# Optimization experiments

Hardware: AMD Instinct MI355X
Metric: run time of the kernel (lower is better)

## Reference

```python
import jax, jax.numpy as jnp
import numpy as np


@jax.custom_vjp
def binarize_ste(x):
    return jnp.sign(x)


def _binarize_fwd(x):
    return jnp.sign(x), None


def _binarize_bwd(_, g):
    # straight-through estimator: pass gradient through, clamped to [-1, 1]
    return (jnp.clip(g, -1.0, 1.0),)


binarize_ste.defvjp(_binarize_fwd, _binarize_bwd)


def setup_inputs() -> dict:
    key = jax.random.key(0)
    kx, kw = jax.random.split(key)
    x = jax.random.normal(kx, (32, 128, 64, 64), dtype=jnp.float32)  # NCHW
    weight = jax.random.normal(kw, (256, 128, 3, 3), dtype=jnp.float32)  # OIHW
    return {"x": x, "weight": weight}


def reference(x, weight):
    w_bin = binarize_ste(weight)  # +/-1 (0 where weight==0, matching torch.sign)
    out = jax.lax.conv_general_dilated(
        x, w_bin,
        window_strides=(1, 1),
        padding=((1, 1), (1, 1)),
        dimension_numbers=("NCHW", "OIHW", "NCHW"),
    )
    return out
```

## Files before the change

### kernel.cpp

```cpp
#include <hip/hip_runtime.h>
#include <hip/hip_bf16.h>


typedef short bf16x8 __attribute__((ext_vector_type(8)));
typedef float f32x4 __attribute__((ext_vector_type(4)));

#define XT_ELEMS (32 * 66 * 66 * 128)
#define XT_BYTES (XT_ELEMS * 2)

__device__ __forceinline__ void glds16(const void* g, const void* l) {
    __builtin_amdgcn_global_load_lds(
        (const __attribute__((address_space(1))) void*)g,
        (__attribute__((address_space(3))) void*)l, 16, 0, 0);
}

__global__ void prep_w_kernel(const float* __restrict__ w,
                              __hip_bfloat16* __restrict__ wm) {
    int tid = blockIdx.x * 256 + threadIdx.x;
    int o = tid / 1152;
    int r = tid - o * 1152;
    int j = r >> 7;
    int c = r & 127;
    float v = w[o * 1152 + c * 9 + j];
    float s = (v > 0.f) ? 1.f : ((v < 0.f) ? -1.f : 0.f);
    wm[tid] = __float2bfloat16(s);
}

__global__ void transpose_x_kernel(const float* __restrict__ x,
                                   __hip_bfloat16* __restrict__ xt) {
    __shared__ short tl[64 * 130];
    const int t = threadIdx.x;
    const int n = blockIdx.x >> 6;
    const int h = blockIdx.x & 63;
    const float* xp = x + (size_t)n * 524288 + h * 64;
    for (int i = t; i < 8192; i += 256) {
        int w = i & 63, c = i >> 6;
        tl[w * 130 + c] = (short)__bfloat16_as_ushort(__float2bfloat16(xp[c * 4096 + w]));
    }
    uint* xtn = (uint*)(xt + (size_t)n * 66 * 66 * 128);
    {
        int row = h + 1;
        if (t < 64)       xtn[(row * 66 + 0) * 64 + t] = 0u;
        else if (t < 128) xtn[(row * 66 + 65) * 64 + (t - 64)] = 0u;
    }
    if (h == 0)  for (int i = t; i < 66 * 64; i += 256) xtn[i] = 0u;
    if (h == 63) for (int i = t; i < 66 * 64; i += 256) xtn[65 * 66 * 64 + i] = 0u;
    __syncthreads();
    uint* xo = (uint*)(xt + ((size_t)(n * 66 + h + 1) * 66 + 1) * 128);
    for (int i = t; i < 4096; i += 256) {
        int c2 = i & 63;
        int w = i >> 6;
        xo[w * 64 + c2] = *(const uint*)(tl + w * 130 + c2 * 2);
    }
}

__global__ __launch_bounds__(256, 2) void gemm_kernel(
    const __hip_bfloat16* __restrict__ xt,
    const __hip_bfloat16* __restrict__ wm,
    float* __restrict__ out) {
    __shared__ short As[128 * 64];
    __shared__ short Bw[2112 * 8];

    const int t = threadIdx.x;
    const int lane = t & 63;
    const int wv = t >> 6;
    const int px_blk = blockIdx.x;
    const int o_blk = blockIdx.y;
    const int n = px_blk >> 4;
    const int h0 = (px_blk & 15) * 4;

    const int wo = (wv & 1) * 64;
    const int wp = (wv >> 1) * 128;
    const int wpr = wp >> 6;
    const int l15 = lane & 15;
    const int quad = lane >> 4;
    const int srow = lane >> 3;
    const int sseg = lane & 7;

    const short* wmS = (const short*)wm + (o_blk * 128) * 1152;
    const short* xtS = (const short*)xt;

    f32x4 acc[4][8] = {};

    for (int cc = 0; cc < 128; cc += 64) {
        for (int kh = 0; kh < 3; ++kh) {
            const short* xw = xtS + ((size_t)(n * 66 + h0 + kh) * 66) * 128;
#pragma unroll
            for (int i = 0; i < 9; ++i) {
                int bidx = i * 4 + wv;
                if (bidx < 33) {
                    int l = bidx * 64 + lane;
                    int cell = l >> 3;
                    int q = l & 7;
                    int s = q ^ (cell & 7);
                    glds16(xw + cell * 128 + cc + s * 8, Bw + bidx * 512);
                }
            }
            for (int kw = 0; kw < 3; ++kw) {
                const int j = kh * 3 + kw;
#pragma unroll
                for (int i = 0; i < 4; ++i) {
                    int r0 = wv * 32 + i * 8;
                    int r = r0 + srow;
                    int segl = sseg ^ (r & 7);
                    glds16(wmS + r * 1152 + j * 128 + cc + segl * 8,
                           As + r0 * 64);
                }
                __syncthreads();
#pragma unroll
                for (int kf = 0; kf < 2; ++kf) {
                    bf16x8 a[4], b[8];
#pragma unroll
                    for (int i = 0; i < 4; ++i) {
                        int o = wo + i * 16 + l15;
                        int seg = (kf * 4 + quad) ^ (o & 7);
                        a[i] = *(const bf16x8*)(As + o * 64 + seg * 8);
                    }
#pragma unroll
                    for (int i = 0; i < 8; ++i) {
                        int cell = (wpr + (i >> 2)) * 66 + (i & 3) * 16 + l15 + kw;
                        int seg = (kf * 4 + quad) ^ (cell & 7);
                        b[i] = *(const bf16x8*)(Bw + cell * 64 + seg * 8);
                    }
#pragma unroll
                    for (int i = 0; i < 4; ++i)
#pragma unroll
                        for (int jj = 0; jj < 8; ++jj)
                            acc[i][jj] = __builtin_amdgcn_mfma_f32_16x16x32_bf16(
                                a[i], b[jj], acc[i][jj], 0, 0, 0);
                }
                __syncthreads();
            }
        }
    }

    const int Pbase = px_blk * 256 + wp;
#pragma unroll
    for (int i = 0; i < 4; ++i) {
#pragma unroll
        for (int jj = 0; jj < 8; ++jj) {
            const int P = Pbase + jj * 16 + l15;
            const int hw = P & 4095;
            float* op = out + (size_t)n * 1048576 + hw;
#pragma unroll
            for (int r = 0; r < 4; ++r) {
                const int o = o_blk * 128 + wo + i * 16 + quad * 4 + r;
                op[(size_t)o * 4096] = acc[i][jj][r];
            }
        }
    }
}

extern "C" void kernel_launch(void* const* d_in, const int* in_sizes, int n_in,
                              void* d_out, int out_size, void* d_ws, size_t ws_size,
                              hipStream_t stream) {
    const float* x = (const float*)d_in[0];
    const float* w = (const float*)d_in[1];
    float* out = (float*)d_out;
    __hip_bfloat16* xt = (__hip_bfloat16*)d_ws;
    __hip_bfloat16* wm = (__hip_bfloat16*)((char*)d_ws + XT_BYTES);

    prep_w_kernel<<<1152, 256, 0, stream>>>(w, wm);
    transpose_x_kernel<<<2048, 256, 0, stream>>>(x, xt);
    gemm_kernel<<<dim3(512, 2), 256, 0, stream>>>(xt, wm, out);
}
```

Baseline: 249.0 us.

## Load weights directly from global into registers and drop LDS A staging

The weight prep kernel now writes binarized weights in a fragment-friendly layout, so each lane can load its MFMA A operand straight from global memory and the LDS As buffer goes away. This removes the per-kw LDS staging of A and two of the three barriers per kh. Block indices are also remapped to change L2 locality across images. In exchange, the global weight loads are now exposed in the inner loop instead of being hidden behind LDS, and each wave fetches its own weights directly, which adds latency risk.

```diff
diff --git a/kernel.cpp b/kernel.cpp
--- a/kernel.cpp
+++ b/kernel.cpp
@@ -17,11 +17,11 @@
 __global__ void prep_w_kernel(const float* __restrict__ w,
                               __hip_bfloat16* __restrict__ wm) {
     int tid = blockIdx.x * 256 + threadIdx.x;
-    int o = tid / 1152;
-    int r = tid - o * 1152;
-    int j = r >> 7;
-    int c = r & 127;
-    float v = w[o * 1152 + c * 9 + j];
+    int e = tid & 7;
+    int o = (tid >> 3) & 255;
+    int c8 = (tid >> 11) & 15;
+    int j = tid >> 15;
+    float v = w[o * 1152 + (c8 * 8 + e) * 9 + j];
     float s = (v > 0.f) ? 1.f : ((v < 0.f) ? -1.f : 0.f);
     wm[tid] = __float2bfloat16(s);
 }
@@ -58,13 +58,16 @@
     const __hip_bfloat16* __restrict__ xt,
     const __hip_bfloat16* __restrict__ wm,
     float* __restrict__ out) {
-    __shared__ short As[128 * 64];
-    __shared__ short Bw[2112 * 8];
+    __shared__ short Bw[264 * 64];
 
     const int t = threadIdx.x;
     const int lane = t & 63;
     const int wv = t >> 6;
-    const int px_blk = blockIdx.x;
+    const int l15 = lane & 15;
+    const int quad = lane >> 4;
+
+    const int bid = blockIdx.x;
+    const int px_blk = (bid & 7) * 64 + (bid >> 3);
     const int o_blk = blockIdx.y;
     const int n = px_blk >> 4;
     const int h0 = (px_blk & 15) * 4;
@@ -72,17 +75,15 @@
     const int wo = (wv & 1) * 64;
     const int wp = (wv >> 1) * 128;
     const int wpr = wp >> 6;
-    const int l15 = lane & 15;
-    const int quad = lane >> 4;
-    const int srow = lane >> 3;
-    const int sseg = lane & 7;
 
-    const short* wmS = (const short*)wm + (o_blk * 128) * 1152;
     const short* xtS = (const short*)xt;
+    const short* aL = (const short*)wm +
+        (size_t)(o_blk * 128 + wo + l15) * 8 + quad * 2048;
 
     f32x4 acc[4][8] = {};
 
     for (int cc = 0; cc < 128; cc += 64) {
+        const int ccA = (cc >> 6) * 8 * 2048;
         for (int kh = 0; kh < 3; ++kh) {
             const short* xw = xtS + ((size_t)(n * 66 + h0 + kh) * 66) * 128;
 #pragma unroll
@@ -96,26 +97,17 @@
                     glds16(xw + cell * 128 + cc + s * 8, Bw + bidx * 512);
                 }
             }
+            __syncthreads();
+#pragma unroll
             for (int kw = 0; kw < 3; ++kw) {
                 const int j = kh * 3 + kw;
-#pragma unroll
-                for (int i = 0; i < 4; ++i) {
-                    int r0 = wv * 32 + i * 8;
-                    int r = r0 + srow;
-                    int segl = sseg ^ (r & 7);
-                    glds16(wmS + r * 1152 + j * 128 + cc + segl * 8,
-                           As + r0 * 64);
-                }
-                __syncthreads();
+                const short* ap = aL + j * 32768 + ccA;
 #pragma unroll
                 for (int kf = 0; kf < 2; ++kf) {
                     bf16x8 a[4], b[8];
 #pragma unroll
-                    for (int i = 0; i < 4; ++i) {
-                        int o = wo + i * 16 + l15;
-                        int seg = (kf * 4 + quad) ^ (o & 7);
-                        a[i] = *(const bf16x8*)(As + o * 64 + seg * 8);
-                    }
+                    for (int i = 0; i < 4; ++i)
+                        a[i] = *(const bf16x8*)(ap + kf * 8192 + i * 128);
 #pragma unroll
                     for (int i = 0; i < 8; ++i) {
                         int cell = (wpr + (i >> 2)) * 66 + (i & 3) * 16 + l15 + kw;
@@ -129,8 +121,8 @@
                             acc[i][jj] = __builtin_amdgcn_mfma_f32_16x16x32_bf16(
                                 a[i], b[jj], acc[i][jj], 0, 0, 0);
                 }
-                __syncthreads();
             }
+            __syncthreads();
         }
     }
 
```

New measurement: 300.1 us. +20.6%, slower.
